# Kernel optimization log

Measured on AMD Instinct MI355X. Metric: run time of the kernel, lower is better.

## Reference

```python
import jax, jax.numpy as jnp
import numpy as np

DIM = 1024
HEADS = 16
DIM_HEAD = 64


def setup_inputs() -> dict:
    key = jax.random.key(0)
    k1, k2 = jax.random.split(key)
    x = jax.random.normal(k1, (2, 2048, DIM), dtype=jnp.float32)
    # to_qkv: Linear(dim, 3*heads*dim_head, bias=False); torch weight is [out,in],
    # we store the transposed [in,out] form for x @ W.
    W_qkv = jax.random.normal(k2, (DIM, 3 * HEADS * DIM_HEAD), dtype=jnp.float32) * (DIM ** -0.5)
    return {"x": x, "W_qkv": W_qkv}


def reference(x, W_qkv):
    b, n, _ = x.shape
    h, d = HEADS, DIM_HEAD
    scale = d ** -0.5
    qkv = x @ W_qkv                              # [b, n, 3*h*d]
    q, k, v = jnp.split(qkv, 3, axis=-1)
    # 'b n (h d) -> b h n d'
    q = q.reshape(b, n, h, d).transpose(0, 2, 1, 3)
    k = k.reshape(b, n, h, d).transpose(0, 2, 1, 3)
    v = v.reshape(b, n, h, d).transpose(0, 2, 1, 3)
    dots = jnp.einsum('bhnd,bhmd->bhnm', q, k) * scale
    attn = jax.nn.softmax(dots, axis=-1)
    out = jnp.einsum('bhnm,bhmd->bhnd', attn, v)
    out = out.transpose(0, 2, 1, 3).reshape(b, n, h * d)  # 'b h n d -> b n (h d)'
    return out + x  # residual (to_out is never applied in the source forward)
```

## Files before the change

kernel.cpp:

```cpp
#include <hip/hip_runtime.h>

#define DIM   1024
#define NQKV  3072
#define SEQ   2048
#define HEADS 16
#define DHEAD 64
#define M_TOT 4096

typedef __bf16 bf16;
typedef __bf16 bf16x8 __attribute__((ext_vector_type(8)));
typedef float  f32x4  __attribute__((ext_vector_type(4)));

typedef const __attribute__((address_space(1))) unsigned int gu32;
typedef __attribute__((address_space(3))) unsigned int su32;

static __device__ __forceinline__ unsigned short f2b(float f) {
    bf16 h = (bf16)f;
    return __builtin_bit_cast(unsigned short, h);
}

#define CAST_BLOCKS (M_TOT * DIM / (256 * 4))
__global__ void prep_kernel(const float* __restrict__ x,
                            unsigned short* __restrict__ xb,
                            const float* __restrict__ W,
                            unsigned short* __restrict__ Wt) {
    __shared__ float tile[32][33];
    const int id  = blockIdx.x;
    const int tid = threadIdx.x;
    if (id < CAST_BLOCKS) {
        int i = (id * 256 + tid) * 4;
        float4 v = *(const float4*)(x + i);
        ushort4 o;
        o.x = f2b(v.x); o.y = f2b(v.y); o.z = f2b(v.z); o.w = f2b(v.w);
        *(ushort4*)(xb + i) = o;
    } else {
        int t  = id - CAST_BLOCKS;
        int nb = t % (NQKV / 32);
        int kb = t / (NQKV / 32);
        int tx = tid & 31, ty0 = tid >> 5;
        for (int ty = ty0; ty < 32; ty += 8)
            tile[ty][tx] = W[(size_t)(kb*32 + ty)*NQKV + nb*32 + tx];
        __syncthreads();
        for (int ty = ty0; ty < 32; ty += 8) {
            int n = nb*32 + ty;
            float s = (n < 1024) ? 0.18033688f : 1.0f;
            Wt[(size_t)n*DIM + kb*32 + tx] = f2b(tile[tx][ty] * s);
        }
    }
}

#define LDC 136
__global__ __launch_bounds__(256) void qkv_gemm_kernel(
    const unsigned short* __restrict__ A,
    const unsigned short* __restrict__ Bt,
    unsigned short* __restrict__ Qw,
    unsigned short* __restrict__ Kw,
    unsigned short* __restrict__ Vtw)
{
    __shared__ __align__(16) unsigned char smem[128 * LDC * 2];
    unsigned short* As = (unsigned short*)smem;
    unsigned short* Bs = (unsigned short*)(smem + 16384);
    unsigned short* Cs = (unsigned short*)smem;

    const int tid  = threadIdx.x;
    const int m0   = blockIdx.y * 128;
    const int n0   = blockIdx.x * 128;
    const int w    = tid >> 6;
    const int lane = tid & 63;
    const int l16  = lane & 15;
    const int quad = lane >> 4;
    const int wm   = (w >> 1) * 64;
    const int wn   = (w & 1) * 64;
    const int srow = lane >> 3;
    const int scol = (lane & 7) * 8;

    f32x4 acc[4][4];
    const f32x4 fzero = {0.f, 0.f, 0.f, 0.f};
    for (int i = 0; i < 4; i++)
        for (int j = 0; j < 4; j++) acc[i][j] = fzero;

    const unsigned short* Ag = A  + (size_t)(m0 + w * 32 + srow) * DIM + scol;
    const unsigned short* Bg = Bt + (size_t)(n0 + w * 32 + srow) * DIM + scol;

    for (int kt = 0; kt < DIM; kt += 64) {
        #pragma unroll
        for (int j = 0; j < 4; j++) {
            __builtin_amdgcn_global_load_lds((gu32*)(Ag + kt + (size_t)j * 8 * DIM),
                                             (su32*)&As[(w * 32 + j * 8) * 64], 16, 0, 0);
            __builtin_amdgcn_global_load_lds((gu32*)(Bg + kt + (size_t)j * 8 * DIM),
                                             (su32*)&Bs[(w * 32 + j * 8) * 64], 16, 0, 0);
        }
        __syncthreads();
        #pragma unroll
        for (int s = 0; s < 2; s++) {
            bf16x8 af[4], bfr[4];
            #pragma unroll
            for (int i = 0; i < 4; i++) {
                af[i]  = *(const bf16x8*)(&As[(wm + i * 16 + l16) * 64 + s * 32 + quad * 8]);
                bfr[i] = *(const bf16x8*)(&Bs[(wn + i * 16 + l16) * 64 + s * 32 + quad * 8]);
            }
            #pragma unroll
            for (int i = 0; i < 4; i++)
                #pragma unroll
                for (int j = 0; j < 4; j++)
                    acc[i][j] = __builtin_amdgcn_mfma_f32_16x16x32_bf16(af[i], bfr[j], acc[i][j], 0, 0, 0);
        }
        __syncthreads();
    }

    const int part = n0 >> 10;
    const int h0   = (n0 & 1023) >> 6;
    const int b    = m0 >> 11;
    const int np0  = m0 & 2047;

    if (part < 2) {
        #pragma unroll
        for (int i = 0; i < 4; i++)
            #pragma unroll
            for (int j = 0; j < 4; j++)
                #pragma unroll
                for (int r = 0; r < 4; r++)
                    Cs[(wm + i * 16 + quad * 4 + r) * LDC + wn + j * 16 + l16] = f2b(acc[i][j][r]);
        __syncthreads();
        unsigned short* dst = (part == 0) ? Qw : Kw;
        #pragma unroll
        for (int pass = 0; pass < 8; pass++) {
            int mi = pass * 16 + (tid >> 4);
            int ci = (tid & 15) * 8;
            uint4 v = *(const uint4*)&Cs[mi * LDC + ci];
            int bh = b * HEADS + h0 + (ci >> 6);
            *(uint4*)&dst[((size_t)bh * SEQ + np0 + mi) * DHEAD + (ci & 63)] = v;
        }
    } else {
        #pragma unroll
        for (int i = 0; i < 4; i++)
            #pragma unroll
            for (int j = 0; j < 4; j++) {
                ushort4 pk;
                pk.x = f2b(acc[i][j][0]); pk.y = f2b(acc[i][j][1]);
                pk.z = f2b(acc[i][j][2]); pk.w = f2b(acc[i][j][3]);
                *(ushort4*)&Cs[(wn + j * 16 + l16) * LDC + wm + i * 16 + quad * 4] = pk;
            }
        __syncthreads();
        #pragma unroll
        for (int pass = 0; pass < 8; pass++) {
            int ci = pass * 16 + (tid >> 4);
            int mi = (tid & 15) * 8;
            uint4 v = *(const uint4*)&Cs[ci * LDC + mi];
            int bh = b * HEADS + h0 + (ci >> 6);
            *(uint4*)&Vtw[((size_t)bh * DHEAD + (ci & 63)) * SEQ + np0 + mi] = v;
        }
    }
}

#define LDK 72
__global__ __launch_bounds__(256) void attn_kernel(
    const unsigned short* __restrict__ Qw,
    const unsigned short* __restrict__ Kw,
    const unsigned short* __restrict__ Vtw,
    const float* __restrict__ x,
    float* __restrict__ out)
{
    __shared__ __align__(16) unsigned short Ks[64 * LDK];
    __shared__ __align__(16) unsigned short Vs[64 * LDK];
    const int id  = blockIdx.x;
    const int qt  = id >> 5;
    const int bh  = ((id & 7) << 2) | ((id >> 3) & 3);
    const int tid = threadIdx.x;
    const int w   = tid >> 6, lane = tid & 63;
    const int l16 = lane & 15, quad = lane >> 4;

    const unsigned short* Qbase = Qw + ((size_t)bh * SEQ + qt * 64 + w * 16 + l16) * DHEAD;
    bf16x8 qf[2];
    qf[0] = *(const bf16x8*)(Qbase + quad * 8);
    qf[1] = *(const bf16x8*)(Qbase + 32 + quad * 8);

    const int prow = ((l16 >> 2) << 3) | (l16 & 3);

    bf16x8 ones;
    #pragma unroll
    for (int j = 0; j < 8; j++) ones[j] = (bf16)1.0f;

    f32x4 o[4], dsum;
    const f32x4 fzero = {0.f, 0.f, 0.f, 0.f};
    #pragma unroll
    for (int d = 0; d < 4; d++) o[d] = fzero;
    dsum = fzero;

    const unsigned short* Kg = Kw  + (size_t)bh * SEQ * DHEAD;
    const unsigned short* Vg = Vtw + (size_t)bh * DHEAD * SEQ;

    const int r0 = tid >> 3, c0 = (tid & 7) * 8;
    uint4 kreg0 = *(const uint4*)(Kg + (size_t)r0 * DHEAD + c0);
    uint4 kreg1 = *(const uint4*)(Kg + (size_t)(r0 + 32) * DHEAD + c0);
    uint4 vreg0 = *(const uint4*)(Vg + (size_t)r0 * SEQ + c0);
    uint4 vreg1 = *(const uint4*)(Vg + (size_t)(r0 + 32) * SEQ + c0);

    for (int t = 0; t < SEQ / 64; t++) {
        __syncthreads();
        *(uint4*)&Ks[r0 * LDK + c0]        = kreg0;
        *(uint4*)&Ks[(r0 + 32) * LDK + c0] = kreg1;
        *(uint4*)&Vs[r0 * LDK + c0]        = vreg0;
        *(uint4*)&Vs[(r0 + 32) * LDK + c0] = vreg1;
        int kvn = ((t + 1) & (SEQ / 64 - 1)) * 64;
        kreg0 = *(const uint4*)(Kg + (size_t)(kvn + r0) * DHEAD + c0);
        kreg1 = *(const uint4*)(Kg + (size_t)(kvn + r0 + 32) * DHEAD + c0);
        vreg0 = *(const uint4*)(Vg + (size_t)r0 * SEQ + kvn + c0);
        vreg1 = *(const uint4*)(Vg + (size_t)(r0 + 32) * SEQ + kvn + c0);
        __syncthreads();

        f32x4 sacc[4];
        #pragma unroll
        for (int ki = 0; ki < 4; ki++) sacc[ki] = fzero;
        #pragma unroll
        for (int s = 0; s < 2; s++)
            #pragma unroll
            for (int ki = 0; ki < 4; ki++) {
                bf16x8 kf = *(const bf16x8*)(
                    &Ks[((ki >> 1) * 32 + prow + (ki & 1) * 4) * LDK + s * 32 + quad * 8]);
                sacc[ki] = __builtin_amdgcn_mfma_f32_16x16x32_bf16(kf, qf[s], sacc[ki], 0, 0, 0);
            }

        bf16x8 pf[2];
        #pragma unroll
        for (int s = 0; s < 2; s++)
            #pragma unroll
            for (int half = 0; half < 2; half++) {
                int ki = 2 * s + half;
                #pragma unroll
                for (int r = 0; r < 4; r++)
                    pf[s][half * 4 + r] = (bf16)__builtin_amdgcn_exp2f(sacc[ki][r]);
            }

        #pragma unroll
        for (int s = 0; s < 2; s++) {
            dsum = __builtin_amdgcn_mfma_f32_16x16x32_bf16(pf[s], ones, dsum, 0, 0, 0);
            #pragma unroll
            for (int d = 0; d < 4; d++) {
                bf16x8 vf = *(const bf16x8*)(&Vs[(d * 16 + l16) * LDK + s * 32 + quad * 8]);
                o[d] = __builtin_amdgcn_mfma_f32_16x16x32_bf16(pf[s], vf, o[d], 0, 0, 0);
            }
        }
    }

    float lr[4];
    #pragma unroll
    for (int r = 0; r < 4; r++) lr[r] = __builtin_amdgcn_rcpf(dsum[r]);

    const int b = bh >> 4, h = bh & 15;
    #pragma unroll
    for (int di = 0; di < 4; di++)
        #pragma unroll
        for (int r = 0; r < 4; r++) {
            int np  = qt * 64 + w * 16 + quad * 4 + r;
            int col = h * 64 + di * 16 + l16;
            size_t g = ((size_t)(b * SEQ + np)) * DIM + col;
            out[g] = o[di][r] * lr[r] + x[g];
        }
}

extern "C" void kernel_launch(void* const* d_in, const int* in_sizes, int n_in,
                              void* d_out, int out_size, void* d_ws, size_t ws_size,
                              hipStream_t stream) {
    const float* x  = (const float*)d_in[0];
    const float* Wq = (const float*)d_in[1];
    float* out = (float*)d_out;

    unsigned short* xb = (unsigned short*)d_ws;
    unsigned short* Wt = xb + (size_t)M_TOT * DIM;
    unsigned short* Qw = Wt + (size_t)NQKV * DIM;
    unsigned short* Kw = Qw + (size_t)32 * SEQ * DHEAD;
    unsigned short* Vt = Kw + (size_t)32 * SEQ * DHEAD;

    prep_kernel<<<CAST_BLOCKS + (NQKV / 32) * (DIM / 32), 256, 0, stream>>>(x, xb, Wq, Wt);
    qkv_gemm_kernel<<<dim3(NQKV / 128, M_TOT / 128), 256, 0, stream>>>(xb, Wt, Qw, Kw, Vt);
    attn_kernel<<<(SEQ / 64) * 32, 256, 0, stream>>>(Qw, Kw, Vt, x, out);
}
```

Baseline: 177.1 us.

## Double-buffer K/V shared tiles with one barrier per iteration and swizzle K columns

The attention loop moves from a single K/V shared buffer with two barriers per tile to a ping-pong pair of buffers. The next tile is written while the current one is consumed, so only one barrier per iteration is needed. K columns are also XOR-style rotated by row group on store and load to reduce LDS bank conflicts on the K fragment reads. This doubles LDS use per block, which may lower occupancy, and the swizzle adds a small amount of index arithmetic.

```diff
diff --git a/kernel.cpp b/kernel.cpp
--- a/kernel.cpp
+++ b/kernel.cpp
@@ -161,8 +161,8 @@
     const float* __restrict__ x,
     float* __restrict__ out)
 {
-    __shared__ __align__(16) unsigned short Ks[64 * LDK];
-    __shared__ __align__(16) unsigned short Vs[64 * LDK];
+    __shared__ __align__(16) unsigned short Ks[2][64 * LDK];
+    __shared__ __align__(16) unsigned short Vs[2][64 * LDK];
     const int id  = blockIdx.x;
     const int qt  = id >> 5;
     const int bh  = ((id & 7) << 2) | ((id >> 3) & 3);
@@ -176,6 +176,8 @@
     qf[1] = *(const bf16x8*)(Qbase + 32 + quad * 8);
 
     const int prow = ((l16 >> 2) << 3) | (l16 & 3);
+    const int co0 = (((quad + 2 * (l16 >> 2)) & 7)) * 8;
+    const int co1 = (((4 + quad + 2 * (l16 >> 2)) & 7)) * 8;
 
     bf16x8 ones;
     #pragma unroll
@@ -191,35 +193,45 @@
     const unsigned short* Vg = Vtw + (size_t)bh * DHEAD * SEQ;
 
     const int r0 = tid >> 3, c0 = (tid & 7) * 8;
+    const int kwc = (((tid & 7) + 2 * (r0 >> 3)) & 7) * 8;
+
     uint4 kreg0 = *(const uint4*)(Kg + (size_t)r0 * DHEAD + c0);
     uint4 kreg1 = *(const uint4*)(Kg + (size_t)(r0 + 32) * DHEAD + c0);
     uint4 vreg0 = *(const uint4*)(Vg + (size_t)r0 * SEQ + c0);
     uint4 vreg1 = *(const uint4*)(Vg + (size_t)(r0 + 32) * SEQ + c0);
+    *(uint4*)&Ks[0][r0 * LDK + kwc]        = kreg0;
+    *(uint4*)&Ks[0][(r0 + 32) * LDK + kwc] = kreg1;
+    *(uint4*)&Vs[0][r0 * LDK + c0]         = vreg0;
+    *(uint4*)&Vs[0][(r0 + 32) * LDK + c0]  = vreg1;
+    kreg0 = *(const uint4*)(Kg + (size_t)(64 + r0) * DHEAD + c0);
+    kreg1 = *(const uint4*)(Kg + (size_t)(64 + r0 + 32) * DHEAD + c0);
+    vreg0 = *(const uint4*)(Vg + (size_t)r0 * SEQ + 64 + c0);
+    vreg1 = *(const uint4*)(Vg + (size_t)(r0 + 32) * SEQ + 64 + c0);
+    __syncthreads();
 
     for (int t = 0; t < SEQ / 64; t++) {
-        __syncthreads();
-        *(uint4*)&Ks[r0 * LDK + c0]        = kreg0;
-        *(uint4*)&Ks[(r0 + 32) * LDK + c0] = kreg1;
-        *(uint4*)&Vs[r0 * LDK + c0]        = vreg0;
-        *(uint4*)&Vs[(r0 + 32) * LDK + c0] = vreg1;
-        int kvn = ((t + 1) & (SEQ / 64 - 1)) * 64;
+        const int cur = t & 1, nxt = cur ^ 1;
+        *(uint4*)&Ks[nxt][r0 * LDK + kwc]        = kreg0;
+        *(uint4*)&Ks[nxt][(r0 + 32) * LDK + kwc] = kreg1;
+        *(uint4*)&Vs[nxt][r0 * LDK + c0]         = vreg0;
+        *(uint4*)&Vs[nxt][(r0 + 32) * LDK + c0]  = vreg1;
+        int kvn = ((t + 2) & (SEQ / 64 - 1)) * 64;
         kreg0 = *(const uint4*)(Kg + (size_t)(kvn + r0) * DHEAD + c0);
         kreg1 = *(const uint4*)(Kg + (size_t)(kvn + r0 + 32) * DHEAD + c0);
         vreg0 = *(const uint4*)(Vg + (size_t)r0 * SEQ + kvn + c0);
         vreg1 = *(const uint4*)(Vg + (size_t)(r0 + 32) * SEQ + kvn + c0);
-        __syncthreads();
 
         f32x4 sacc[4];
         #pragma unroll
         for (int ki = 0; ki < 4; ki++) sacc[ki] = fzero;
         #pragma unroll
-        for (int s = 0; s < 2; s++)
-            #pragma unroll
-            for (int ki = 0; ki < 4; ki++) {
-                bf16x8 kf = *(const bf16x8*)(
-                    &Ks[((ki >> 1) * 32 + prow + (ki & 1) * 4) * LDK + s * 32 + quad * 8]);
-                sacc[ki] = __builtin_amdgcn_mfma_f32_16x16x32_bf16(kf, qf[s], sacc[ki], 0, 0, 0);
-            }
+        for (int ki = 0; ki < 4; ki++) {
+            int row = (ki >> 1) * 32 + prow + (ki & 1) * 4;
+            bf16x8 kf0 = *(const bf16x8*)(&Ks[cur][row * LDK + co0]);
+            sacc[ki] = __builtin_amdgcn_mfma_f32_16x16x32_bf16(kf0, qf[0], sacc[ki], 0, 0, 0);
+            bf16x8 kf1 = *(const bf16x8*)(&Ks[cur][row * LDK + co1]);
+            sacc[ki] = __builtin_amdgcn_mfma_f32_16x16x32_bf16(kf1, qf[1], sacc[ki], 0, 0, 0);
+        }
 
         bf16x8 pf[2];
         #pragma unroll
@@ -237,10 +249,11 @@
             dsum = __builtin_amdgcn_mfma_f32_16x16x32_bf16(pf[s], ones, dsum, 0, 0, 0);
             #pragma unroll
             for (int d = 0; d < 4; d++) {
-                bf16x8 vf = *(const bf16x8*)(&Vs[(d * 16 + l16) * LDK + s * 32 + quad * 8]);
+                bf16x8 vf = *(const bf16x8*)(&Vs[cur][(d * 16 + l16) * LDK + s * 32 + quad * 8]);
                 o[d] = __builtin_amdgcn_mfma_f32_16x16x32_bf16(pf[s], vf, o[d], 0, 0, 0);
             }
         }
+        __syncthreads();
     }
 
     float lr[4];
```

Measured after the change: 179.5 us. Within noise of the previous version (+1.4%).

## Double-buffer K/V tiles in attention and remap GEMM blocks per XCD

Applied to the files above, without the earlier changes.

The attention kernel now keeps two LDS buffers for K and V. The next tile is written while the current one is consumed, which removes one of the two block barriers per iteration. The QKV GEMM launch changes to a 1D grid whose block index is remapped so each XCD handles a contiguous group of three N-tiles, with the aim of improving L2 locality of the weight tiles. The cost is double the LDS in attention, which may reduce occupancy.

```diff
diff --git a/kernel.cpp b/kernel.cpp
--- a/kernel.cpp
+++ b/kernel.cpp
@@ -63,8 +63,11 @@
     unsigned short* Cs = (unsigned short*)smem;
 
     const int tid  = threadIdx.x;
-    const int m0   = blockIdx.y * 128;
-    const int n0   = blockIdx.x * 128;
+    const int id   = blockIdx.x;
+    const int xcd  = id & 7;
+    const int slot = id >> 3;
+    const int m0   = (slot / 3) * 128;
+    const int n0   = (xcd * 3 + slot % 3) * 128;
     const int w    = tid >> 6;
     const int lane = tid & 63;
     const int l16  = lane & 15;
@@ -161,8 +164,8 @@
     const float* __restrict__ x,
     float* __restrict__ out)
 {
-    __shared__ __align__(16) unsigned short Ks[64 * LDK];
-    __shared__ __align__(16) unsigned short Vs[64 * LDK];
+    __shared__ __align__(16) unsigned short Ks[2][64 * LDK];
+    __shared__ __align__(16) unsigned short Vs[2][64 * LDK];
     const int id  = blockIdx.x;
     const int qt  = id >> 5;
     const int bh  = ((id & 7) << 2) | ((id >> 3) & 3);
@@ -191,23 +194,32 @@
     const unsigned short* Vg = Vtw + (size_t)bh * DHEAD * SEQ;
 
     const int r0 = tid >> 3, c0 = (tid & 7) * 8;
+
     uint4 kreg0 = *(const uint4*)(Kg + (size_t)r0 * DHEAD + c0);
     uint4 kreg1 = *(const uint4*)(Kg + (size_t)(r0 + 32) * DHEAD + c0);
     uint4 vreg0 = *(const uint4*)(Vg + (size_t)r0 * SEQ + c0);
     uint4 vreg1 = *(const uint4*)(Vg + (size_t)(r0 + 32) * SEQ + c0);
+    *(uint4*)&Ks[0][r0 * LDK + c0]        = kreg0;
+    *(uint4*)&Ks[0][(r0 + 32) * LDK + c0] = kreg1;
+    *(uint4*)&Vs[0][r0 * LDK + c0]        = vreg0;
+    *(uint4*)&Vs[0][(r0 + 32) * LDK + c0] = vreg1;
+    kreg0 = *(const uint4*)(Kg + (size_t)(64 + r0) * DHEAD + c0);
+    kreg1 = *(const uint4*)(Kg + (size_t)(64 + r0 + 32) * DHEAD + c0);
+    vreg0 = *(const uint4*)(Vg + (size_t)r0 * SEQ + 64 + c0);
+    vreg1 = *(const uint4*)(Vg + (size_t)(r0 + 32) * SEQ + 64 + c0);
+    __syncthreads();
 
     for (int t = 0; t < SEQ / 64; t++) {
-        __syncthreads();
-        *(uint4*)&Ks[r0 * LDK + c0]        = kreg0;
-        *(uint4*)&Ks[(r0 + 32) * LDK + c0] = kreg1;
-        *(uint4*)&Vs[r0 * LDK + c0]        = vreg0;
-        *(uint4*)&Vs[(r0 + 32) * LDK + c0] = vreg1;
-        int kvn = ((t + 1) & (SEQ / 64 - 1)) * 64;
+        const int cur = t & 1, nxt = cur ^ 1;
+        *(uint4*)&Ks[nxt][r0 * LDK + c0]        = kreg0;
+        *(uint4*)&Ks[nxt][(r0 + 32) * LDK + c0] = kreg1;
+        *(uint4*)&Vs[nxt][r0 * LDK + c0]        = vreg0;
+        *(uint4*)&Vs[nxt][(r0 + 32) * LDK + c0] = vreg1;
+        int kvn = ((t + 2) & (SEQ / 64 - 1)) * 64;
         kreg0 = *(const uint4*)(Kg + (size_t)(kvn + r0) * DHEAD + c0);
         kreg1 = *(const uint4*)(Kg + (size_t)(kvn + r0 + 32) * DHEAD + c0);
         vreg0 = *(const uint4*)(Vg + (size_t)r0 * SEQ + kvn + c0);
         vreg1 = *(const uint4*)(Vg + (size_t)(r0 + 32) * SEQ + kvn + c0);
-        __syncthreads();
 
         f32x4 sacc[4];
         #pragma unroll
@@ -217,7 +229,7 @@
             #pragma unroll
             for (int ki = 0; ki < 4; ki++) {
                 bf16x8 kf = *(const bf16x8*)(
-                    &Ks[((ki >> 1) * 32 + prow + (ki & 1) * 4) * LDK + s * 32 + quad * 8]);
+                    &Ks[cur][((ki >> 1) * 32 + prow + (ki & 1) * 4) * LDK + s * 32 + quad * 8]);
                 sacc[ki] = __builtin_amdgcn_mfma_f32_16x16x32_bf16(kf, qf[s], sacc[ki], 0, 0, 0);
             }
 
@@ -237,10 +249,11 @@
             dsum = __builtin_amdgcn_mfma_f32_16x16x32_bf16(pf[s], ones, dsum, 0, 0, 0);
             #pragma unroll
             for (int d = 0; d < 4; d++) {
-                bf16x8 vf = *(const bf16x8*)(&Vs[(d * 16 + l16) * LDK + s * 32 + quad * 8]);
+                bf16x8 vf = *(const bf16x8*)(&Vs[cur][(d * 16 + l16) * LDK + s * 32 + quad * 8]);
                 o[d] = __builtin_amdgcn_mfma_f32_16x16x32_bf16(pf[s], vf, o[d], 0, 0, 0);
             }
         }
+        __syncthreads();
     }
 
     float lr[4];
@@ -273,6 +286,6 @@
     unsigned short* Vt = Kw + (size_t)32 * SEQ * DHEAD;
 
     prep_kernel<<<CAST_BLOCKS + (NQKV / 32) * (DIM / 32), 256, 0, stream>>>(x, xb, Wq, Wt);
-    qkv_gemm_kernel<<<dim3(NQKV / 128, M_TOT / 128), 256, 0, stream>>>(xb, Wt, Qw, Kw, Vt);
+    qkv_gemm_kernel<<<768, 256, 0, stream>>>(xb, Wt, Qw, Kw, Vt);
     attn_kernel<<<(SEQ / 64) * 32, 256, 0, stream>>>(Qw, Kw, Vt, x, out);
 }
```

Result: no change. 177.8 us (+0.4%).
